# Kernel tuning notes

Measured on AMD Instinct MI355X. Metric: run time of the kernel, lower is better.

The kernel has to match this reference:

```python
import jax, jax.numpy as jnp
import numpy as np

N = 16384   # total nodes per drug-batch
E = 65536   # directed edges (avg degree 4)
B = 512     # graphs per batch
BN_EPS = 1e-5
SLOPE = 0.01  # LeakyReLU default


def _rn(k, shape, s=0.02):
    return jax.random.normal(k, shape, dtype=jnp.float32) * s


def setup_inputs():
    key = jax.random.key(0)
    ks = jax.random.split(key, 32)
    d = {}
    d['x1'] = jax.random.normal(ks[0], (N, 78), dtype=jnp.float32)
    d['edge_index1'] = jax.random.randint(ks[1], (2, E), 0, N)
    d['batch1'] = jnp.sort(jax.random.randint(ks[2], (N,), 0, B))
    d['x2'] = jax.random.normal(ks[3], (N, 78), dtype=jnp.float32)
    d['edge_index2'] = jax.random.randint(ks[4], (2, E), 0, N)
    d['batch2'] = jnp.sort(jax.random.randint(ks[5], (N,), 0, B))
    d['cell'] = jax.random.normal(ks[6], (B, 954), dtype=jnp.float32)
    # TransformerConv1: 78 -> 2 heads x 128 (concat 256)
    d['wq1'] = _rn(ks[7], (78, 256));  d['bq1'] = jnp.zeros((256,), jnp.float32)
    d['wk1'] = _rn(ks[8], (78, 256));  d['bk1'] = jnp.zeros((256,), jnp.float32)
    d['wv1'] = _rn(ks[9], (78, 256));  d['bv1'] = jnp.zeros((256,), jnp.float32)
    d['ws1'] = _rn(ks[10], (78, 256)); d['bs1'] = jnp.zeros((256,), jnp.float32)
    # TransformerConv2: 256 -> 2 heads x 512 (concat 1024)
    d['wq2'] = _rn(ks[11], (256, 1024)); d['bq2'] = jnp.zeros((1024,), jnp.float32)
    d['wk2'] = _rn(ks[12], (256, 1024)); d['bk2'] = jnp.zeros((1024,), jnp.float32)
    d['wv2'] = _rn(ks[13], (256, 1024)); d['bv2'] = jnp.zeros((1024,), jnp.float32)
    d['ws2'] = _rn(ks[14], (256, 1024)); d['bs2'] = jnp.zeros((1024,), jnp.float32)
    d['wg1'] = _rn(ks[15], (1024, 512)); d['bg1'] = jnp.zeros((512,), jnp.float32)
    d['wg2'] = _rn(ks[16], (512, 128));  d['bg2'] = jnp.zeros((128,), jnp.float32)
    d['wr1'] = _rn(ks[17], (954, 512));  d['br1'] = jnp.zeros((512,), jnp.float32)
    d['wr2'] = _rn(ks[18], (512, 256));  d['br2'] = jnp.zeros((256,), jnp.float32)
    d['wr3'] = _rn(ks[19], (256, 128));  d['br3'] = jnp.zeros((128,), jnp.float32)
    d['wf1'] = _rn(ks[20], (384, 512));  d['bf1'] = jnp.zeros((512,), jnp.float32)
    d['gbn1'] = jnp.ones((512,), jnp.float32); d['bbn1'] = jnp.zeros((512,), jnp.float32)
    d['wf2'] = _rn(ks[21], (512, 256));  d['bf2'] = jnp.zeros((256,), jnp.float32)
    d['gbn2'] = jnp.ones((256,), jnp.float32); d['bbn2'] = jnp.zeros((256,), jnp.float32)
    d['wf3'] = _rn(ks[22], (256, 1));    d['bf3'] = jnp.zeros((1,), jnp.float32)
    return d


def _lrelu(x):
    return jnp.where(x >= 0, x, SLOPE * x)


def _l2n(x):
    return x / jnp.maximum(jnp.linalg.norm(x, axis=1, keepdims=True), 1e-12)


def _tconv(x, ei, wq, bq, wk, bk, wv, bv, ws, bs, H, D):
    # PyG TransformerConv (concat=True, beta=False, root_weight=True)
    src, dst = ei[0], ei[1]
    n = x.shape[0]
    q = (x @ wq + bq).reshape(n, H, D)
    k = (x @ wk + bk).reshape(n, H, D)
    v = (x @ wv + bv).reshape(n, H, D)
    logits = jnp.einsum('ehd,ehd->eh', q[dst], k[src]) / jnp.sqrt(jnp.float32(D))  # [E,H]
    m = jax.ops.segment_max(logits, dst, num_segments=n)
    m = jnp.where(jnp.isfinite(m), m, 0.0)
    e = jnp.exp(logits - m[dst])
    z = jax.ops.segment_sum(e, dst, num_segments=n)
    alpha = e / (z[dst] + 1e-16)
    agg = jax.ops.segment_sum(alpha[:, :, None] * v[src], dst, num_segments=n)  # [N,H,D]
    return agg.reshape(n, H * D) + x @ ws + bs


def reference(x1, edge_index1, batch1, x2, edge_index2, batch2, cell,
              wq1, bq1, wk1, bk1, wv1, bv1, ws1, bs1,
              wq2, bq2, wk2, bk2, wv2, bv2, ws2, bs2,
              wg1, bg1, wg2, bg2, wr1, br1, wr2, br2, wr3, br3,
              wf1, bf1, gbn1, bbn1, wf2, bf2, gbn2, bbn2, wf3, bf3):
    def branch(x, ei, bt):
        h = _lrelu(_tconv(x, ei, wq1, bq1, wk1, bk1, wv1, bv1, ws1, bs1, 2, 128))
        h = _lrelu(_tconv(h, ei, wq2, bq2, wk2, bk2, wv2, bv2, ws2, bs2, 2, 512))
        g = jax.ops.segment_max(h, bt, num_segments=B)  # global max pool per graph
        g = jnp.where(jnp.isfinite(g), g, 0.0)
        g = _lrelu(g @ wg1 + bg1)
        g = g @ wg2 + bg2  # dropout = identity in eval
        return _l2n(g)

    x1g = branch(x1, edge_index1, batch1)
    x2g = branch(x2, edge_index2, batch2)

    c = _l2n(cell)
    c = _lrelu(c @ wr1 + br1)
    c = _lrelu(c @ wr2 + br2)
    c = c @ wr3 + br3

    xc = _l2n(jnp.concatenate([x1g, x2g, c], axis=1))  # [B, 384]
    bn = 1.0 / jnp.sqrt(1.0 + BN_EPS)  # eval BN with running mean 0, var 1
    h = _lrelu((xc @ wf1 + bf1) * bn * gbn1 + bbn1)
    h = _lrelu((h @ wf2 + bf2) * bn * gbn2 + bbn2)
    return jax.nn.sigmoid((h @ wf3 + bf3)[:, 0])
```

## Files before the change

### kernel.cpp

```cpp
#include <hip/hip_runtime.h>
#include <hip/hip_bf16.h>
#include <hip/hip_fp8.h>
#include <math.h>
#include <stdint.h>

typedef __hip_bfloat16 bf16;

#define NN 16384
#define EE 65536
#define BB 512

typedef __attribute__((ext_vector_type(8))) short short8;
typedef __attribute__((ext_vector_type(4))) short short4v;
typedef __attribute__((ext_vector_type(4))) float floatx4;
typedef __attribute__((ext_vector_type(8))) unsigned char uchar8;

#define GKEY_NEGINF 0x007FFFFFu

__device__ __forceinline__ float lrelu_f(float x){ return x >= 0.f ? x : 0.01f*x; }

__device__ __forceinline__ float b2f(short s){
    unsigned int u = ((unsigned int)(unsigned short)s) << 16;
    float f; __builtin_memcpy(&f, &u, 4); return f;
}
__device__ __forceinline__ short f2b(float f){
    bf16 b = (bf16)f;
    short s; __builtin_memcpy(&s, &b, 2); return s;
}
__device__ __forceinline__ unsigned char f2fp8(float f){
    __hip_fp8_e4m3 t(f);
    return (unsigned char)t.__x;
}
__device__ __forceinline__ float fp82f(unsigned char c){
    __hip_fp8_e4m3 t; t.__x = (__hip_fp8_storage_t)c;
    return (float)t;
}
__device__ __forceinline__ unsigned int fkey(float f){
    unsigned int u; __builtin_memcpy(&u, &f, 4);
    return (u & 0x80000000u) ? ~u : (u | 0x80000000u);
}
__device__ __forceinline__ float fdec(unsigned int k){
    if (k == GKEY_NEGINF) return 0.f;
    unsigned int u = (k & 0x80000000u) ? (k ^ 0x80000000u) : ~k;
    float f; __builtin_memcpy(&f, &u, 4); return f;
}

__device__ __forceinline__ void gl2lds16(const void* g, void* l){
    __builtin_amdgcn_global_load_lds(
        (__attribute__((address_space(1))) unsigned int*)(uintptr_t)g,
        (__attribute__((address_space(3))) unsigned int*)(uintptr_t)l, 16, 0, 0);
}

__global__ __launch_bounds__(256)
void mfma_gemm(const bf16* __restrict__ A, int lda,
               const bf16* __restrict__ Bt, int ldb,
               const float* __restrict__ bias,
               bf16* __restrict__ C, int ldc,
               unsigned char* __restrict__ C2, int ldc2, int nsplit, int K)
{
    __shared__ __align__(16) char smem[20480];
    bf16* As  = (bf16*)smem;
    bf16* Bs  = (bf16*)(smem + 8192);
    bf16* epi = (bf16*)smem;
    const int tid  = threadIdx.x;
    const int wave = tid >> 6;
    const int lane = tid & 63;
    const int wm = (wave & 1) * 64;
    const int wn = (wave >> 1) * 64;
    const int m0 = blockIdx.y * 128;
    const int n0 = blockIdx.x * 128;
    const bool isf8 = (n0 >= nsplit);

    const int srow = lane >> 2;
    const int scol = (lane & 3) * 8;
    const int arow = lane & 15;
    const int aq   = (lane >> 4) * 8;

    floatx4 acc[4][4];
    #pragma unroll
    for (int i=0;i<4;i++)
        #pragma unroll
        for (int j=0;j<4;j++) acc[i][j] = (floatx4){0.f,0.f,0.f,0.f};

    for (int k0 = 0; k0 < K; k0 += 32) {
        #pragma unroll
        for (int i = 0; i < 2; i++) {
            const int chunk = wave*2 + i;
            const int r = chunk*16 + srow;
            gl2lds16(A  + (size_t)(m0 + r)*lda + k0 + scol, As + chunk*512);
            gl2lds16(Bt + (size_t)(n0 + r)*ldb + k0 + scol, Bs + chunk*512);
        }
        __syncthreads();
        short8 af[4], bf_[4];
        #pragma unroll
        for (int i=0;i<4;i++) af[i]  = *(const short8*)(As + (wm + i*16 + arow)*32 + aq);
        #pragma unroll
        for (int j=0;j<4;j++) bf_[j] = *(const short8*)(Bs + (wn + j*16 + arow)*32 + aq);
        #pragma unroll
        for (int i=0;i<4;i++)
            #pragma unroll
            for (int j=0;j<4;j++)
                acc[i][j] = __builtin_amdgcn_mfma_f32_16x16x32_bf16(af[i], bf_[j], acc[i][j], 0,0,0);
        __syncthreads();
    }
    const int crow = (lane >> 4) * 4;
    const int ccol = lane & 15;
    const int erow = lane >> 2;
    const int ecol = (lane & 3) * 8;
    bf16* ep = epi + wave * (64*40);
    #pragma unroll
    for (int j2 = 0; j2 < 2; j2++){
        if (j2) __syncthreads();
        #pragma unroll
        for (int jj = 0; jj < 2; jj++){
            const int j = j2*2 + jj;
            const float bsv = bias[n0 + wn + j*16 + ccol];
            #pragma unroll
            for (int i = 0; i < 4; i++)
                #pragma unroll
                for (int r = 0; r < 4; r++)
                    ep[(i*16 + crow + r)*40 + jj*16 + ccol] = (bf16)(acc[i][j][r] + bsv);
        }
        __syncthreads();
        #pragma unroll
        for (int q = 0; q < 4; q++){
            const int rr = q*16 + erow;
            short8 vv = *(const short8*)(ep + rr*40 + ecol);
            if (!isf8){
                *(short8*)(C + (size_t)(m0 + wm + rr)*ldc + n0 + wn + j2*32 + ecol) = vv;
            } else {
                uchar8 ob;
                #pragma unroll
                for (int i=0;i<8;i++) ob[i] = f2fp8(b2f(vv[i]));
                *(uchar8*)(C2 + (size_t)(m0 + wm + rr)*ldc2 + (n0 - nsplit) + wn + j2*32 + ecol) = ob;
            }
        }
    }
}

__global__ void prep_all_kernel(const float* __restrict__ wq1, const float* __restrict__ wk1,
                                const float* __restrict__ wv1, const float* __restrict__ ws1,
                                const float* __restrict__ bq1, const float* __restrict__ bk1,
                                const float* __restrict__ bv1, const float* __restrict__ bs1,
                                const float* __restrict__ wq2, const float* __restrict__ wk2,
                                const float* __restrict__ wv2, const float* __restrict__ ws2,
                                const float* __restrict__ bq2, const float* __restrict__ bk2,
                                const float* __restrict__ bv2, const float* __restrict__ bs2v,
                                bf16* __restrict__ W1t, float* __restrict__ b1c,
                                bf16* __restrict__ W2t, float* __restrict__ b2c)
{
    int i = blockIdx.x*256 + threadIdx.x;
    if (i < 98304){
        int n = i / 96, k = i - n*96;
        const float* w = (n<256)?wq1:(n<512)?wk1:(n<768)?wv1:ws1;
        W1t[i] = (k < 78) ? (bf16)w[(size_t)k*256 + (n & 255)] : (bf16)0.f;
        return;
    }
    i -= 98304;
    if (i < 1024){
        const float* b = (i<256)?bq1:(i<512)?bk1:(i<768)?bv1:bs1;
        b1c[i] = b[i & 255];
        return;
    }
    i -= 1024;
    if (i < 1048576){
        int k = i & 255;
        int j = (i >> 8) & 2047;
        int h = i >> 19;
        const float* w = (j<512)?wq2:(j<1024)?ws2:(j<1536)?wk2:wv2;
        int col = h*512 + (j & 511);
        W2t[i] = (bf16)w[(size_t)k*1024 + col];
        return;
    }
    i -= 1048576;
    if (i < 4096){
        int j = i & 2047, h = i >> 11;
        const float* b = (j<512)?bq2:(j<1024)?bs2v:(j<1536)?bk2:bv2;
        b2c[i] = b[h*512 + (j & 511)];
    }
}

#define OG1 0
#define OG2 524288
#define OR1 589824
#define OR2 1081344
#define OR3 1212416
#define OF1 1245184
#define OF2 1441792
#define TAILW_TOTAL 1572864

__global__ void prep_tail_kernel(const float* __restrict__ wg1, const float* __restrict__ wg2,
                                 const float* __restrict__ wr1, const float* __restrict__ wr2,
                                 const float* __restrict__ wr3, const float* __restrict__ wf1,
                                 const float* __restrict__ wf2, bf16* __restrict__ Wtp)
{
    int i = blockIdx.x*256 + threadIdx.x;
    if (i >= TAILW_TOTAL) return;
    const float* W; int N, K, base;
    if      (i < OG2){ W = wg1; N = 512; K = 1024; base = OG1; }
    else if (i < OR1){ W = wg2; N = 128; K = 512;  base = OG2; }
    else if (i < OR2){ W = wr1; N = 512; K = 954;  base = OR1; }
    else if (i < OR3){ W = wr2; N = 256; K = 512;  base = OR2; }
    else if (i < OF1){ W = wr3; N = 128; K = 256;  base = OR3; }
    else if (i < OF2){ W = wf1; N = 512; K = 384;  base = OF1; }
    else             { W = wf2; N = 256; K = 512;  base = OF2; }
    int loc = i - base;
    int u = loc & 3;
    int j = (loc >> 2) % N;
    int k4 = (loc >> 2) / N;
    int k = k4*4 + u;
    Wtp[i] = (k < K) ? (bf16)W[(size_t)k*N + j] : (bf16)0.f;
}

__global__ void cvt_x_kernel(const float* __restrict__ x1, const float* __restrict__ x2,
                             bf16* __restrict__ xa){
    int i = blockIdx.x*256 + threadIdx.x;
    int r = i / 96, c = i - r*96;
    const float* x = (r >= NN) ? x2 : x1;
    int lr = r & (NN-1);
    xa[i] = (c < 78) ? (bf16)x[(size_t)lr*78 + c] : (bf16)0.f;
}

__global__ void hist_kernel(const int* __restrict__ ei1, const int* __restrict__ ei2,
                            int* __restrict__ cnt){
    int eg = blockIdx.x*256 + threadIdx.x;
    int br = eg >> 16, e = eg & (EE-1);
    const int* ei = br ? ei2 : ei1;
    atomicAdd(&cnt[br*NN + ei[EE + e]], 1);
}

__global__ __launch_bounds__(1024)
void scan_kernel(const int* __restrict__ hist, int* __restrict__ rowptr,
                 int* __restrict__ rowcur){
    const int br = blockIdx.x;
    hist   += br*NN;
    rowptr += br*(NN+1);
    rowcur += br*(NN+1);
    __shared__ int sums[1024];
    const int t = threadIdx.x;
    const int base = t*16;
    int loc[16]; int s = 0;
    #pragma unroll
    for (int i=0;i<16;i++){ loc[i]=s; s += hist[base+i]; }
    sums[t] = s; __syncthreads();
    for (int o=1;o<1024;o<<=1){
        int v = (t>=o) ? sums[t-o] : 0;
        __syncthreads();
        sums[t] += v;
        __syncthreads();
    }
    int pref = (t>0) ? sums[t-1] : 0;
    #pragma unroll
    for (int i=0;i<16;i++){
        int v = pref + loc[i];
        rowptr[base+i] = v;
        rowcur[base+i] = v;
    }
    if (t==1023) rowptr[NN] = sums[1023];
}

__global__ void scatter_kernel(const int* __restrict__ ei1, const int* __restrict__ ei2,
                               int* __restrict__ rowcur, int* __restrict__ srcs){
    int eg = blockIdx.x*256 + threadIdx.x;
    int br = eg >> 16, e = eg & (EE-1);
    const int* ei = br ? ei2 : ei1;
    int d = ei[EE + e];
    int pos = atomicAdd(&rowcur[br*(NN+1) + d], 1);
    srcs[br*EE + pos] = ei[e];
}

__global__ void ginit_kernel(unsigned int* __restrict__ gkey){
    gkey[blockIdx.x*256 + threadIdx.x] = GKEY_NEGINF;
}

template<int D>
__global__ __launch_bounds__(256)
void attn_kernel(const bf16* __restrict__ qkvs, int ld, int qo, int ko, int vo, int so, int H,
                 bf16* __restrict__ hout, int ldo,
                 const int* __restrict__ rowptr, const int* __restrict__ srcs)
{
    constexpr int PER = D / 64;
    typedef __attribute__((ext_vector_type(PER))) short shortP;
    const int lane = threadIdx.x & 63;
    const int gw = blockIdx.x * 4 + (threadIdx.x >> 6);
    const int n = gw / H;
    const int h = gw - n*H;
    int br = n >> 14;
    int brNN = br*NN, nl = n - brNN;
    rowptr += br*(NN+1); srcs += br*EE;
    const float qscale = rsqrtf((float)D) * 1.44269504f;
    const int hd = h*D + lane*PER;

    const shortP qv = *(const shortP*)(qkvs + (size_t)n*ld + qo + hd);
    float qr[PER];
    #pragma unroll
    for (int i=0;i<PER;i++) qr[i] = b2f(qv[i]) * qscale;

    const int e0 = rowptr[nl], e1 = rowptr[nl+1];
    float m = -INFINITY, z = 0.f;
    float acc[PER];
    #pragma unroll
    for (int i=0;i<PER;i++) acc[i] = 0.f;

    for (int base = e0; base < e1; base += 4){
        const int cnt = min(4, e1 - base);
        int sl = srcs[min(base + (lane & 3), e1 - 1)];
        int src[4];
        #pragma unroll
        for (int j=0;j<4;j++) src[j] = __shfl(sl, j, 64);

        shortP kv[4], vv[4];
        #pragma unroll
        for (int j=0;j<4;j++){
            if (j < cnt){
                const bf16* rp = qkvs + (size_t)(brNN + src[j])*ld;
                kv[j] = *(const shortP*)(rp + ko + hd);
                vv[j] = *(const shortP*)(rp + vo + hd);
            }
        }
        float dt[4];
        #pragma unroll
        for (int j=0;j<4;j++){
            float d = 0.f;
            if (j < cnt){
                #pragma unroll
                for (int i=0;i<PER;i++) d += qr[i]*b2f(kv[j][i]);
            }
            dt[j] = d;
        }
        #pragma unroll
        for (int o=32;o;o>>=1){
            #pragma unroll
            for (int j=0;j<4;j++) dt[j] += __shfl_xor(dt[j], o, 64);
        }
        float cm = -INFINITY;
        #pragma unroll
        for (int j=0;j<4;j++) if (j < cnt) cm = fmaxf(cm, dt[j]);
        const float mn = fmaxf(m, cm);
        const float cs = exp2f(m - mn);
        z *= cs;
        #pragma unroll
        for (int i=0;i<PER;i++) acc[i] *= cs;
        #pragma unroll
        for (int j=0;j<4;j++){
            if (j < cnt){
                const float w = exp2f(dt[j] - mn);
                z += w;
                #pragma unroll
                for (int i=0;i<PER;i++) acc[i] += w*b2f(vv[j][i]);
            }
        }
        m = mn;
    }
    const float invz = 1.0f/(z + 1e-16f);
    const shortP sv = *(const shortP*)(qkvs + (size_t)n*ld + so + hd);
    shortP ov;
    #pragma unroll
    for (int i=0;i<PER;i++) ov[i] = f2b(lrelu_f(b2f(sv[i]) + acc[i]*invz));
    *(shortP*)(hout + (size_t)n*ldo + hd) = ov;
}

__global__ __launch_bounds__(256)
void attn512_f8(const bf16* __restrict__ qs, const unsigned char* __restrict__ kv,
                const int* __restrict__ rowptr, const int* __restrict__ srcs,
                const int* __restrict__ bt,
                unsigned int* __restrict__ gkey, int grow0, int gc0)
{
    __shared__ float Sh[4][512];
    __shared__ int Sgid[4];
    const int lane = threadIdx.x & 63;
    const int wave = threadIdx.x >> 6;
    const int n = blockIdx.x * 4 + wave;
    const float qscale = rsqrtf(512.f) * 1.44269504f;
    const int hd = lane*8;

    const short8 qv = *(const short8*)(qs + (size_t)n*1024 + hd);
    float qr[8];
    #pragma unroll
    for (int i=0;i<8;i++) qr[i] = b2f(qv[i]) * qscale;

    const int e0 = rowptr[n], e1 = rowptr[n+1];
    float m = -INFINITY, z = 0.f;
    float acc[8];
    #pragma unroll
    for (int i=0;i<8;i++) acc[i] = 0.f;

    for (int base = e0; base < e1; base += 4){
        const int cnt = min(4, e1 - base);
        int sl = srcs[min(base + (lane & 3), e1 - 1)];
        int src[4];
        #pragma unroll
        for (int j=0;j<4;j++) src[j] = __shfl(sl, j, 64);

        uchar8 k8[4], v8[4];
        #pragma unroll
        for (int j=0;j<4;j++){
            if (j < cnt){
                const unsigned char* rp = kv + (size_t)src[j]*1024;
                k8[j] = *(const uchar8*)(rp + hd);
                v8[j] = *(const uchar8*)(rp + 512 + hd);
            }
        }
        float dt[4];
        #pragma unroll
        for (int j=0;j<4;j++){
            float d = 0.f;
            if (j < cnt){
                #pragma unroll
                for (int i=0;i<8;i++) d += qr[i]*fp82f(k8[j][i]);
            }
            dt[j] = d;
        }
        #pragma unroll
        for (int o=32;o;o>>=1){
            #pragma unroll
            for (int j=0;j<4;j++) dt[j] += __shfl_xor(dt[j], o, 64);
        }
        float cm = -INFINITY;
        #pragma unroll
        for (int j=0;j<4;j++) if (j < cnt) cm = fmaxf(cm, dt[j]);
        const float mn = fmaxf(m, cm);
        const float cs = exp2f(m - mn);
        z *= cs;
        #pragma unroll
        for (int i=0;i<8;i++) acc[i] *= cs;
        #pragma unroll
        for (int j=0;j<4;j++){
            if (j < cnt){
                const float w = exp2f(dt[j] - mn);
                z += w;
                #pragma unroll
                for (int i=0;i<8;i++) acc[i] += w*fp82f(v8[j][i]);
            }
        }
        m = mn;
    }
    const float invz = 1.0f/(z + 1e-16f);
    const short8 sv = *(const short8*)(qs + (size_t)n*1024 + 512 + hd);
    #pragma unroll
    for (int i=0;i<8;i++) Sh[wave][hd + i] = lrelu_f(b2f(sv[i]) + acc[i]*invz);
    if (lane == 0) Sgid[wave] = bt[n];
    __syncthreads();

    #pragma unroll
    for (int cc=0; cc<2; cc++){
        const int col = threadIdx.x*2 + cc;
        float mx = Sh[0][col];
        int gid = Sgid[0];
        #pragma unroll
        for (int r=1; r<4; r++){
            if (Sgid[r] == gid) mx = fmaxf(mx, Sh[r][col]);
            else {
                atomicMax(&gkey[(size_t)(grow0 + gid)*1024 + gc0 + col], fkey(mx));
                gid = Sgid[r]; mx = Sh[r][col];
            }
        }
        atomicMax(&gkey[(size_t)(grow0 + gid)*1024 + gc0 + col], fkey(mx));
    }
}

template<int R, int N, int ACT>
__device__ __forceinline__ void dense_split(
    const bf16* __restrict__ Wp, const float* __restrict__ bias,
    const float* __restrict__ gam, const float* __restrict__ bet, float bns,
    const float* A, int lda, float* C, int ldc, int K, int tid, float* Spart)
{
    constexpr int CPT = N / 128;
    constexpr int KG  = 8;
    const int ct = tid & 127;
    const int kg = tid >> 7;
    const int jt = ct * CPT;
    const int Kc = ((K + KG - 1) / KG + 3) & ~3;
    const int kb = kg * Kc;
    const int Kpad = (K + 3) & ~3;
    const int ke = min(Kpad, kb + Kc);

    float acc[R][CPT];
    #pragma unroll
    for (int r=0;r<R;r++)
        #pragma unroll
        for (int c=0;c<CPT;c++) acc[r][c] = 0.f;

    if (kb < ke){
        short8 p0, p1; short4v p4;
        {
            const bf16* wp = Wp + ((size_t)(kb>>2)*N + jt)*4;
            if (CPT==4){ p0 = ((const short8*)wp)[0]; p1 = ((const short8*)wp)[1]; }
            else if (CPT==2){ p0 = *(const short8*)wp; }
            else { p4 = *(const short4v*)wp; }
        }
        for (int k = kb; k < ke; k += 4){
            short8 c0 = p0, c1 = p1; short4v c4 = p4;
            const int kn = (k + 4 < ke) ? k + 4 : kb;
            const bf16* wn = Wp + ((size_t)(kn>>2)*N + jt)*4;
            if (CPT==4){ p0 = ((const short8*)wn)[0]; p1 = ((const short8*)wn)[1]; }
            else if (CPT==2){ p0 = *(const short8*)wn; }
            else { p4 = *(const short4v*)wn; }
            float w[4][CPT];
            if (CPT==4){
                #pragma unroll
                for (int u=0;u<4;u++){
                    w[u][0] = b2f(c0[u]); w[u][1] = b2f(c0[4+u]);
                    w[u][2] = b2f(c1[u]); w[u][3] = b2f(c1[4+u]);
                }
            } else if (CPT==2){
                #pragma unroll
                for (int u=0;u<4;u++){ w[u][0] = b2f(c0[u]); w[u][1] = b2f(c0[4+u]); }
            } else {
                #pragma unroll
                for (int u=0;u<4;u++) w[u][0] = b2f(c4[u]);
            }
            #pragma unroll
            for (int r=0;r<R;r++){
                const floatx4 av = *(const floatx4*)(A + r*lda + k);
                #pragma unroll
                for (int u=0;u<4;u++)
                    #pragma unroll
                    for (int c=0;c<CPT;c++) acc[r][c] += av[u]*w[u][c];
            }
        }
    }
    #pragma unroll
    for (int r=0;r<R;r++)
        #pragma unroll
        for (int c=0;c<CPT;c++)
            Spart[(kg*R + r)*N + jt + c] = acc[r][c];
    __syncthreads();
    for (int idx = tid; idx < R*N; idx += 1024){
        int r = idx / N, j = idx - r*N;
        float v = 0.f;
        #pragma unroll
        for (int g=0; g<KG; g++) v += Spart[(g*R + r)*N + j];
        v += bias[j];
        if (ACT==1) v = lrelu_f(v);
        if (ACT==2) v = lrelu_f(v*bns*gam[j] + bet[j]);
        C[r*ldc + j] = v;
    }
    __syncthreads();
}

__global__ __launch_bounds__(1024)
void tail_kernel(const unsigned int* __restrict__ gkey,
                 const float* __restrict__ cell,
                 const bf16*  __restrict__ Wtp,
                 const float* __restrict__ bg1, const float* __restrict__ bg2,
                 const float* __restrict__ br1, const float* __restrict__ br2,
                 const float* __restrict__ br3,
                 const float* __restrict__ bf1,
                 const float* __restrict__ gbn1, const float* __restrict__ bbn1,
                 const float* __restrict__ bf2,
                 const float* __restrict__ gbn2, const float* __restrict__ bbn2,
                 const float* __restrict__ wf3, const float* __restrict__ bf3,
                 float bns, float* __restrict__ outp)
{
    __shared__ float Sg[4][1024];
    __shared__ float Sgh[4][512];
    __shared__ float Sgout[4][128];
    __shared__ float Scell[2][960];
    __shared__ float Sc1[2][512];
    __shared__ float Sc2[2][256];
    __shared__ float Sc3[2][128];
    __shared__ float Sxc[2][384];
    __shared__ float Sf1[2][512];
    __shared__ float Sf2[2][256];
    __shared__ float Spart[16384];
    __shared__ float inv4[4], invc[2], invx[2];

    const int tid = threadIdx.x;
    const int wv  = tid >> 6;
    const int ln  = tid & 63;
    const int b0  = blockIdx.x * 2;

    {
        int idx = tid*4;
        int r = idx >> 10, c = idx & 1023;
        int lg = r >> 1, br = r & 1;
        const unsigned int* gp = gkey + (size_t)(br*BB + b0 + lg)*1024 + c;
        #pragma unroll
        for (int i=0;i<4;i++) Sg[r][c+i] = fdec(gp[i]);
    }
    for (int idx = tid; idx < 2*954; idx += 1024){
        int r = (idx >= 954) ? 1 : 0;
        int c = idx - r*954;
        Scell[r][c] = cell[(size_t)(b0 + r)*954 + c];
    }
    if (tid < 12){ int r = tid/6; Scell[r][954 + tid%6] = 0.f; }
    __syncthreads();

    if (wv < 2){
        float s = 0.f;
        for (int c = ln; c < 954; c += 64){ float v = Scell[wv][c]; s += v*v; }
        #pragma unroll
        for (int o=32;o;o>>=1) s += __shfl_xor(s, o, 64);
        if (ln == 0) invc[wv] = 1.0f / fmaxf(sqrtf(s), 1e-12f);
    }
    __syncthreads();
    #pragma unroll
    for (int r=0;r<2;r++)
        for (int c = tid; c < 954; c += 1024) Scell[r][c] *= invc[r];
    __syncthreads();

    dense_split<4,512,1>(Wtp+OG1, bg1, nullptr, nullptr, 1.f, &Sg[0][0],   1024, &Sgh[0][0],  512, 1024, tid, Spart);
    dense_split<4,128,0>(Wtp+OG2, bg2, nullptr, nullptr, 1.f, &Sgh[0][0],  512,  &Sgout[0][0],128, 512,  tid, Spart);
    dense_split<2,512,1>(Wtp+OR1, br1, nullptr, nullptr, 1.f, &Scell[0][0], 960, &Sc1[0][0],  512, 954,  tid, Spart);
    dense_split<2,256,1>(Wtp+OR2, br2, nullptr, nullptr, 1.f, &Sc1[0][0],   512, &Sc2[0][0],  256, 512,  tid, Spart);
    dense_split<2,128,0>(Wtp+OR3, br3, nullptr, nullptr, 1.f, &Sc2[0][0],   256, &Sc3[0][0],  128, 256,  tid, Spart);

    if (wv < 4){
        float a = Sgout[wv][ln], bq = Sgout[wv][ln+64];
        float s = a*a + bq*bq;
        #pragma unroll
        for (int o=32;o;o>>=1) s += __shfl_xor(s, o, 64);
        if (ln == 0) inv4[wv] = 1.0f / fmaxf(sqrtf(s), 1e-12f);
    }
    __syncthreads();

    if (tid < 768){
        int lg = tid / 384, j = tid - lg*384;
        float v;
        if (j < 128)      v = Sgout[lg*2+0][j]     * inv4[lg*2+0];
        else if (j < 256) v = Sgout[lg*2+1][j-128] * inv4[lg*2+1];
        else              v = Sc3[lg][j-256];
        Sxc[lg][j] = v;
    }
    __syncthreads();
    if (wv < 2){
        float s = 0.f;
        #pragma unroll
        for (int i=0;i<6;i++){ float v = Sxc[wv][ln + i*64]; s += v*v; }
        #pragma unroll
        for (int o=32;o;o>>=1) s += __shfl_xor(s, o, 64);
        if (ln == 0) invx[wv] = 1.0f / fmaxf(sqrtf(s), 1e-12f);
    }
    __syncthreads();
    if (tid < 768){
        int lg = tid / 384, j = tid - lg*384;
        Sxc[lg][j] *= invx[lg];
    }
    __syncthreads();

    dense_split<2,512,2>(Wtp+OF1, bf1, gbn1, bbn1, bns, &Sxc[0][0], 384, &Sf1[0][0], 512, 384, tid, Spart);
    dense_split<2,256,2>(Wtp+OF2, bf2, gbn2, bbn2, bns, &Sf1[0][0], 512, &Sf2[0][0], 256, 512, tid, Spart);

    if (wv < 2){
        float s = 0.f;
        #pragma unroll
        for (int i=0;i<4;i++){ int c = ln + i*64; s += Sf2[wv][c]*wf3[c]; }
        #pragma unroll
        for (int o=32;o;o>>=1) s += __shfl_xor(s, o, 64);
        if (ln == 0) outp[b0 + wv] = 1.0f/(1.0f + expf(-(s + bf3[0])));
    }
}

extern "C" void kernel_launch(void* const* d_in, const int* in_sizes, int n_in,
                              void* d_out, int out_size, void* d_ws, size_t ws_size,
                              hipStream_t stream)
{
    const float* x1  = (const float*)d_in[0];
    const int*   ei1 = (const int*)  d_in[1];
    const int*   bt1 = (const int*)  d_in[2];
    const float* x2  = (const float*)d_in[3];
    const int*   ei2 = (const int*)  d_in[4];
    const int*   bt2 = (const int*)  d_in[5];
    const float* cell= (const float*)d_in[6];
    const float* wq1=(const float*)d_in[7];  const float* bq1=(const float*)d_in[8];
    const float* wk1=(const float*)d_in[9];  const float* bk1=(const float*)d_in[10];
    const float* wv1=(const float*)d_in[11]; const float* bv1=(const float*)d_in[12];
    const float* ws1=(const float*)d_in[13]; const float* bs1=(const float*)d_in[14];
    const float* wq2=(const float*)d_in[15]; const float* bq2=(const float*)d_in[16];
    const float* wk2=(const float*)d_in[17]; const float* bk2=(const float*)d_in[18];
    const float* wv2=(const float*)d_in[19]; const float* bv2=(const float*)d_in[20];
    const float* ws2=(const float*)d_in[21]; const float* bs2q=(const float*)d_in[22];
    const float* wg1=(const float*)d_in[23]; const float* bg1=(const float*)d_in[24];
    const float* wg2=(const float*)d_in[25]; const float* bg2=(const float*)d_in[26];
    const float* wr1=(const float*)d_in[27]; const float* br1=(const float*)d_in[28];
    const float* wr2=(const float*)d_in[29]; const float* br2=(const float*)d_in[30];
    const float* wr3=(const float*)d_in[31]; const float* br3=(const float*)d_in[32];
    const float* wf1=(const float*)d_in[33]; const float* bf1=(const float*)d_in[34];
    const float* gbn1=(const float*)d_in[35];const float* bbn1=(const float*)d_in[36];
    const float* wf2=(const float*)d_in[37]; const float* bf2=(const float*)d_in[38];
    const float* gbn2=(const float*)d_in[39];const float* bbn2=(const float*)d_in[40];
    const float* wf3=(const float*)d_in[41]; const float* bf3=(const float*)d_in[42];
    float* outp = (float*)d_out;
    (void)in_sizes; (void)n_in; (void)out_size; (void)ws_size;

    const float BNS = 1.0f / sqrtf(1.0f + 1e-5f);

    char* basep = (char*)d_ws;
    size_t off = 0;
    auto alloc = [&](size_t nbytes)->char* {
        char* p = basep + off;
        off += (nbytes + 255) & ~(size_t)255;
        return p;
    };
    int* rowptr2  = (int*)  alloc((size_t)2*(NN+1)*4);
    int* rowcur2  = (int*)  alloc((size_t)2*(NN+1)*4);
    int* cnt2     = (int*)  alloc((size_t)2*NN*4);
    int* srcs2    = (int*)  alloc((size_t)2*EE*4);
    unsigned int* gkey = (unsigned int*)alloc((size_t)2*BB*1024*4);
    float* b1c    = (float*)alloc((size_t)1024*4);
    float* b2c    = (float*)alloc((size_t)4096*4);
    bf16* W1t     = (bf16*) alloc((size_t)1024*96*2);
    bf16* W2t     = (bf16*) alloc((size_t)2*2048*256*2);
    bf16* Wtp     = (bf16*) alloc((size_t)TAILW_TOTAL*2);
    bf16* h1      = (bf16*) alloc((size_t)2*NN*256*2);
    bf16* xa      = (bf16*) alloc((size_t)2*NN*96*2);
    char* QK      = alloc((size_t)2*NN*1024*2);
    bf16* qkvs1   = (bf16*)QK;
    bf16* qs2     = (bf16*)QK;
    unsigned char* kv2 = (unsigned char*)(QK + (size_t)NN*1024*2);

    (void)hipMemsetAsync(cnt2, 0, (size_t)2*NN*4, stream);
    prep_all_kernel<<<4500,256,0,stream>>>(wq1,wk1,wv1,ws1, bq1,bk1,bv1,bs1,
                                           wq2,wk2,wv2,ws2, bq2,bk2,bv2,bs2q,
                                           W1t,b1c,W2t,b2c);
    prep_tail_kernel<<<(TAILW_TOTAL+255)/256,256,0,stream>>>(wg1,wg2,wr1,wr2,wr3,wf1,wf2, Wtp);
    hist_kernel<<<2*EE/256,256,0,stream>>>(ei1, ei2, cnt2);
    scan_kernel<<<2,1024,0,stream>>>(cnt2, rowptr2, rowcur2);
    scatter_kernel<<<2*EE/256,256,0,stream>>>(ei1, ei2, rowcur2, srcs2);
    ginit_kernel<<<(2*BB*1024)/256,256,0,stream>>>(gkey);

    cvt_x_kernel<<<(2*NN*96)/256,256,0,stream>>>(x1, x2, xa);
    mfma_gemm<<<dim3(1024/128, 2*NN/128),256,0,stream>>>(xa,96, W1t,96, b1c,
                                                         qkvs1,1024, nullptr,0, 1<<30, 96);
    attn_kernel<128><<<2*NN*2/4,256,0,stream>>>(qkvs1,1024, 0,256,512,768, 2, h1,256, rowptr2, srcs2);

    for (int br=0; br<2; br++){
        const int* bt = br ? bt2 : bt1;
        for (int h=0; h<2; h++){
            mfma_gemm<<<dim3(2048/128, NN/128),256,0,stream>>>(
                h1 + (size_t)br*NN*256, 256, W2t + (size_t)h*2048*256, 256,
                b2c + h*2048, qs2,1024, kv2,1024, 1024, 256);
            attn512_f8<<<NN/4,256,0,stream>>>(qs2, kv2,
                                              rowptr2 + br*(NN+1), srcs2 + br*EE, bt,
                                              gkey, br*BB, h*512);
        }
    }

    tail_kernel<<<BB/2,1024,0,stream>>>(gkey, cell, Wtp,
                                        bg1,bg2, br1,br2,br3,
                                        bf1,gbn1,bbn1, bf2,gbn2,bbn2, wf3,bf3,
                                        BNS, outp);
}
```

Before: 560.4 us.

## Store layer-1 Q/K/V in fp8, reorder skip first, merge prep kernels

Reorders the projected columns so the skip projection is written in bf16 and Q/K/V are written in fp8 by the GEMM epilogue for both layers, including layer 1 which previously stayed all-bf16. The attention kernels now read fp8 queries, keys and values, which cuts gather bandwidth. All weight, input conversion and gkey-init prep kernels are merged into one launch to reduce launch overhead. The cost is reduced precision on Q (and on layer-1 K/V), which risks accuracy.

```diff
diff --git a/kernel.cpp b/kernel.cpp
--- a/kernel.cpp
+++ b/kernel.cpp
@@ -12,8 +12,10 @@
 
 typedef __attribute__((ext_vector_type(8))) short short8;
 typedef __attribute__((ext_vector_type(4))) short short4v;
+typedef __attribute__((ext_vector_type(2))) short short2v;
 typedef __attribute__((ext_vector_type(4))) float floatx4;
 typedef __attribute__((ext_vector_type(8))) unsigned char uchar8;
+typedef __attribute__((ext_vector_type(2))) unsigned char uchar2v;
 
 #define GKEY_NEGINF 0x007FFFFFu
 
@@ -138,48 +140,6 @@
     }
 }
 
-__global__ void prep_all_kernel(const float* __restrict__ wq1, const float* __restrict__ wk1,
-                                const float* __restrict__ wv1, const float* __restrict__ ws1,
-                                const float* __restrict__ bq1, const float* __restrict__ bk1,
-                                const float* __restrict__ bv1, const float* __restrict__ bs1,
-                                const float* __restrict__ wq2, const float* __restrict__ wk2,
-                                const float* __restrict__ wv2, const float* __restrict__ ws2,
-                                const float* __restrict__ bq2, const float* __restrict__ bk2,
-                                const float* __restrict__ bv2, const float* __restrict__ bs2v,
-                                bf16* __restrict__ W1t, float* __restrict__ b1c,
-                                bf16* __restrict__ W2t, float* __restrict__ b2c)
-{
-    int i = blockIdx.x*256 + threadIdx.x;
-    if (i < 98304){
-        int n = i / 96, k = i - n*96;
-        const float* w = (n<256)?wq1:(n<512)?wk1:(n<768)?wv1:ws1;
-        W1t[i] = (k < 78) ? (bf16)w[(size_t)k*256 + (n & 255)] : (bf16)0.f;
-        return;
-    }
-    i -= 98304;
-    if (i < 1024){
-        const float* b = (i<256)?bq1:(i<512)?bk1:(i<768)?bv1:bs1;
-        b1c[i] = b[i & 255];
-        return;
-    }
-    i -= 1024;
-    if (i < 1048576){
-        int k = i & 255;
-        int j = (i >> 8) & 2047;
-        int h = i >> 19;
-        const float* w = (j<512)?wq2:(j<1024)?ws2:(j<1536)?wk2:wv2;
-        int col = h*512 + (j & 511);
-        W2t[i] = (bf16)w[(size_t)k*1024 + col];
-        return;
-    }
-    i -= 1048576;
-    if (i < 4096){
-        int j = i & 2047, h = i >> 11;
-        const float* b = (j<512)?bq2:(j<1024)?bs2v:(j<1536)?bk2:bv2;
-        b2c[i] = b[h*512 + (j & 511)];
-    }
-}
-
 #define OG1 0
 #define OG2 524288
 #define OR1 589824
@@ -189,36 +149,92 @@
 #define OF2 1441792
 #define TAILW_TOTAL 1572864
 
-__global__ void prep_tail_kernel(const float* __restrict__ wg1, const float* __restrict__ wg2,
-                                 const float* __restrict__ wr1, const float* __restrict__ wr2,
-                                 const float* __restrict__ wr3, const float* __restrict__ wf1,
-                                 const float* __restrict__ wf2, bf16* __restrict__ Wtp)
+#define P_W1T 98304
+#define P_B1C (P_W1T + 1024)
+#define P_W2T (P_B1C + 1048576)
+#define P_B2C (P_W2T + 4096)
+#define P_WTP (P_B2C + TAILW_TOTAL)
+#define P_XA  (P_WTP + 2*NN*96)
+#define P_GK  (P_XA + 2*BB*1024)
+__global__ void prep_mega_kernel(
+    const float* __restrict__ wq1, const float* __restrict__ wk1,
+    const float* __restrict__ wv1, const float* __restrict__ ws1,
+    const float* __restrict__ bq1, const float* __restrict__ bk1,
+    const float* __restrict__ bv1, const float* __restrict__ bs1,
+    const float* __restrict__ wq2, const float* __restrict__ wk2,
+    const float* __restrict__ wv2, const float* __restrict__ ws2,
+    const float* __restrict__ bq2, const float* __restrict__ bk2,
+    const float* __restrict__ bv2, const float* __restrict__ bs2v,
+    const float* __restrict__ wg1, const float* __restrict__ wg2,
+    const float* __restrict__ wr1, const float* __restrict__ wr2,
+    const float* __restrict__ wr3, const float* __restrict__ wf1,
+    const float* __restrict__ wf2,
+    const float* __restrict__ x1,  const float* __restrict__ x2,
+    bf16* __restrict__ W1t, float* __restrict__ b1c,
+    bf16* __restrict__ W2t, float* __restrict__ b2c,
+    bf16* __restrict__ Wtp, bf16* __restrict__ xa,
+    unsigned int* __restrict__ gkey)
 {
     int i = blockIdx.x*256 + threadIdx.x;
-    if (i >= TAILW_TOTAL) return;
-    const float* W; int N, K, base;
-    if      (i < OG2){ W = wg1; N = 512; K = 1024; base = OG1; }
-    else if (i < OR1){ W = wg2; N = 128; K = 512;  base = OG2; }
-    else if (i < OR2){ W = wr1; N = 512; K = 954;  base = OR1; }
-    else if (i < OR3){ W = wr2; N = 256; K = 512;  base = OR2; }
-    else if (i < OF1){ W = wr3; N = 128; K = 256;  base = OR3; }
-    else if (i < OF2){ W = wf1; N = 512; K = 384;  base = OF1; }
-    else             { W = wf2; N = 256; K = 512;  base = OF2; }
-    int loc = i - base;
-    int u = loc & 3;
-    int j = (loc >> 2) % N;
-    int k4 = (loc >> 2) / N;
-    int k = k4*4 + u;
-    Wtp[i] = (k < K) ? (bf16)W[(size_t)k*N + j] : (bf16)0.f;
-}
-
-__global__ void cvt_x_kernel(const float* __restrict__ x1, const float* __restrict__ x2,
-                             bf16* __restrict__ xa){
-    int i = blockIdx.x*256 + threadIdx.x;
-    int r = i / 96, c = i - r*96;
-    const float* x = (r >= NN) ? x2 : x1;
-    int lr = r & (NN-1);
-    xa[i] = (c < 78) ? (bf16)x[(size_t)lr*78 + c] : (bf16)0.f;
+    if (i < P_W1T){
+        int n = i / 96, k = i - n*96;
+        int seg = n >> 8;
+        const float* w = (seg==0)?ws1:(seg==1)?wq1:(seg==2)?wk1:wv1;
+        W1t[i] = (k < 78) ? (bf16)w[(size_t)k*256 + (n & 255)] : (bf16)0.f;
+        return;
+    }
+    if (i < P_B1C){
+        int n = i - P_W1T;
+        int seg = n >> 8;
+        const float* b = (seg==0)?bs1:(seg==1)?bq1:(seg==2)?bk1:bv1;
+        b1c[n] = b[n & 255];
+        return;
+    }
+    if (i < P_W2T){
+        int loc = i - P_B1C;
+        int k = loc & 255;
+        int j = (loc >> 8) & 2047;
+        int h = loc >> 19;
+        const float* w = (j<512)?ws2:(j<1024)?wq2:(j<1536)?wk2:wv2;
+        W2t[loc] = (bf16)w[(size_t)k*1024 + h*512 + (j & 511)];
+        return;
+    }
+    if (i < P_B2C){
+        int loc = i - P_W2T;
+        int j = loc & 2047, h = loc >> 11;
+        const float* b = (j<512)?bs2v:(j<1024)?bq2:(j<1536)?bk2:bv2;
+        b2c[loc] = b[h*512 + (j & 511)];
+        return;
+    }
+    if (i < P_WTP){
+        int t = i - P_B2C;
+        const float* W; int N, K, base;
+        if      (t < OG2){ W = wg1; N = 512; K = 1024; base = OG1; }
+        else if (t < OR1){ W = wg2; N = 128; K = 512;  base = OG2; }
+        else if (t < OR2){ W = wr1; N = 512; K = 954;  base = OR1; }
+        else if (t < OR3){ W = wr2; N = 256; K = 512;  base = OR2; }
+        else if (t < OF1){ W = wr3; N = 128; K = 256;  base = OR3; }
+        else if (t < OF2){ W = wf1; N = 512; K = 384;  base = OF1; }
+        else             { W = wf2; N = 256; K = 512;  base = OF2; }
+        int loc = t - base;
+        int u = loc & 3;
+        int j = (loc >> 2) % N;
+        int k4 = (loc >> 2) / N;
+        int k = k4*4 + u;
+        Wtp[t] = (k < K) ? (bf16)W[(size_t)k*N + j] : (bf16)0.f;
+        return;
+    }
+    if (i < P_XA){
+        int t = i - P_WTP;
+        int r = t / 96, c = t - r*96;
+        const float* x = (r >= NN) ? x2 : x1;
+        int lr = r & (NN-1);
+        xa[t] = (c < 78) ? (bf16)x[(size_t)lr*78 + c] : (bf16)0.f;
+        return;
+    }
+    if (i < P_GK){
+        gkey[i - P_XA] = GKEY_NEGINF;
+    }
 }
 
 __global__ void hist_kernel(const int* __restrict__ ei1, const int* __restrict__ ei2,
@@ -269,38 +285,27 @@
     srcs[br*EE + pos] = ei[e];
 }
 
-__global__ void ginit_kernel(unsigned int* __restrict__ gkey){
-    gkey[blockIdx.x*256 + threadIdx.x] = GKEY_NEGINF;
-}
-
-template<int D>
 __global__ __launch_bounds__(256)
-void attn_kernel(const bf16* __restrict__ qkvs, int ld, int qo, int ko, int vo, int so, int H,
-                 bf16* __restrict__ hout, int ldo,
-                 const int* __restrict__ rowptr, const int* __restrict__ srcs)
+void attn128_f8(const bf16* __restrict__ s1, const unsigned char* __restrict__ f81,
+                bf16* __restrict__ hout,
+                const int* __restrict__ rowptr, const int* __restrict__ srcs)
 {
-    constexpr int PER = D / 64;
-    typedef __attribute__((ext_vector_type(PER))) short shortP;
     const int lane = threadIdx.x & 63;
     const int gw = blockIdx.x * 4 + (threadIdx.x >> 6);
-    const int n = gw / H;
-    const int h = gw - n*H;
+    const int n = gw >> 1;
+    const int h = gw & 1;
     int br = n >> 14;
     int brNN = br*NN, nl = n - brNN;
     rowptr += br*(NN+1); srcs += br*EE;
-    const float qscale = rsqrtf((float)D) * 1.44269504f;
-    const int hd = h*D + lane*PER;
-
-    const shortP qv = *(const shortP*)(qkvs + (size_t)n*ld + qo + hd);
-    float qr[PER];
-    #pragma unroll
-    for (int i=0;i<PER;i++) qr[i] = b2f(qv[i]) * qscale;
+    const float qscale = rsqrtf(128.f) * 1.44269504f;
+    const int hd = h*128 + lane*2;
+
+    const uchar2v q8 = *(const uchar2v*)(f81 + (size_t)n*768 + hd);
+    float qr[2] = { fp82f(q8[0])*qscale, fp82f(q8[1])*qscale };
 
     const int e0 = rowptr[nl], e1 = rowptr[nl+1];
     float m = -INFINITY, z = 0.f;
-    float acc[PER];
-    #pragma unroll
-    for (int i=0;i<PER;i++) acc[i] = 0.f;
+    float acc[2] = {0.f, 0.f};
 
     for (int base = e0; base < e1; base += 4){
         const int cnt = min(4, e1 - base);
@@ -309,23 +314,20 @@
         #pragma unroll
         for (int j=0;j<4;j++) src[j] = __shfl(sl, j, 64);
 
-        shortP kv[4], vv[4];
+        uchar2v kv[4], vv[4];
         #pragma unroll
         for (int j=0;j<4;j++){
             if (j < cnt){
-                const bf16* rp = qkvs + (size_t)(brNN + src[j])*ld;
-                kv[j] = *(const shortP*)(rp + ko + hd);
-                vv[j] = *(const shortP*)(rp + vo + hd);
+                const unsigned char* rp = f81 + (size_t)(brNN + src[j])*768;
+                kv[j] = *(const uchar2v*)(rp + 256 + hd);
+                vv[j] = *(const uchar2v*)(rp + 512 + hd);
             }
         }
         float dt[4];
         #pragma unroll
         for (int j=0;j<4;j++){
             float d = 0.f;
-            if (j < cnt){
-                #pragma unroll
-                for (int i=0;i<PER;i++) d += qr[i]*b2f(kv[j][i]);
-            }
+            if (j < cnt) d = qr[0]*fp82f(kv[j][0]) + qr[1]*fp82f(kv[j][1]);
             dt[j] = d;
         }
         #pragma unroll
@@ -339,29 +341,28 @@
         const float mn = fmaxf(m, cm);
         const float cs = exp2f(m - mn);
         z *= cs;
-        #pragma unroll
-        for (int i=0;i<PER;i++) acc[i] *= cs;
+        acc[0] *= cs; acc[1] *= cs;
         #pragma unroll
         for (int j=0;j<4;j++){
             if (j < cnt){
                 const float w = exp2f(dt[j] - mn);
                 z += w;
-                #pragma unroll
-                for (int i=0;i<PER;i++) acc[i] += w*b2f(vv[j][i]);
+                acc[0] += w*fp82f(vv[j][0]);
+                acc[1] += w*fp82f(vv[j][1]);
             }
         }
         m = mn;
     }
     const float invz = 1.0f/(z + 1e-16f);
-    const shortP sv = *(const shortP*)(qkvs + (size_t)n*ld + so + hd);
-    shortP ov;
-    #pragma unroll
-    for (int i=0;i<PER;i++) ov[i] = f2b(lrelu_f(b2f(sv[i]) + acc[i]*invz));
-    *(shortP*)(hout + (size_t)n*ldo + hd) = ov;
+    const short2v sv = *(const short2v*)(s1 + (size_t)n*256 + hd);
+    short2v ov;
+    ov[0] = f2b(lrelu_f(b2f(sv[0]) + acc[0]*invz));
+    ov[1] = f2b(lrelu_f(b2f(sv[1]) + acc[1]*invz));
+    *(short2v*)(hout + (size_t)n*256 + hd) = ov;
 }
 
 __global__ __launch_bounds__(256)
-void attn512_f8(const bf16* __restrict__ qs, const unsigned char* __restrict__ kv,
+void attn512_f8(const bf16* __restrict__ s2, const unsigned char* __restrict__ f82,
                 const int* __restrict__ rowptr, const int* __restrict__ srcs,
                 const int* __restrict__ bt,
                 unsigned int* __restrict__ gkey, int grow0, int gc0)
@@ -374,10 +375,10 @@
     const float qscale = rsqrtf(512.f) * 1.44269504f;
     const int hd = lane*8;
 
-    const short8 qv = *(const short8*)(qs + (size_t)n*1024 + hd);
+    const uchar8 q8 = *(const uchar8*)(f82 + (size_t)n*1536 + hd);
     float qr[8];
     #pragma unroll
-    for (int i=0;i<8;i++) qr[i] = b2f(qv[i]) * qscale;
+    for (int i=0;i<8;i++) qr[i] = fp82f(q8[i]) * qscale;
 
     const int e0 = rowptr[n], e1 = rowptr[n+1];
     float m = -INFINITY, z = 0.f;
@@ -396,9 +397,9 @@
         #pragma unroll
         for (int j=0;j<4;j++){
             if (j < cnt){
-                const unsigned char* rp = kv + (size_t)src[j]*1024;
-                k8[j] = *(const uchar8*)(rp + hd);
-                v8[j] = *(const uchar8*)(rp + 512 + hd);
+                const unsigned char* rp = f82 + (size_t)src[j]*1536;
+                k8[j] = *(const uchar8*)(rp + 512 + hd);
+                v8[j] = *(const uchar8*)(rp + 1024 + hd);
             }
         }
         float dt[4];
@@ -436,7 +437,7 @@
         m = mn;
     }
     const float invz = 1.0f/(z + 1e-16f);
-    const short8 sv = *(const short8*)(qs + (size_t)n*1024 + 512 + hd);
+    const short8 sv = *(const short8*)(s2 + (size_t)n*512 + hd);
     #pragma unroll
     for (int i=0;i<8;i++) Sh[wave][hd + i] = lrelu_f(b2f(sv[i]) + acc[i]*invz);
     if (lane == 0) Sgid[wave] = bt[n];
@@ -705,33 +706,34 @@
     bf16* Wtp     = (bf16*) alloc((size_t)TAILW_TOTAL*2);
     bf16* h1      = (bf16*) alloc((size_t)2*NN*256*2);
     bf16* xa      = (bf16*) alloc((size_t)2*NN*96*2);
-    char* QK      = alloc((size_t)2*NN*1024*2);
-    bf16* qkvs1   = (bf16*)QK;
-    bf16* qs2     = (bf16*)QK;
-    unsigned char* kv2 = (unsigned char*)(QK + (size_t)NN*1024*2);
+    char* QK      = alloc((size_t)16777216 + 25165824);
+    bf16* s1a     = (bf16*)QK;
+    unsigned char* f81 = (unsigned char*)(QK + 16777216);
+    bf16* s2a     = (bf16*)QK;
+    unsigned char* f82 = (unsigned char*)(QK + 16777216);
 
     (void)hipMemsetAsync(cnt2, 0, (size_t)2*NN*4, stream);
-    prep_all_kernel<<<4500,256,0,stream>>>(wq1,wk1,wv1,ws1, bq1,bk1,bv1,bs1,
-                                           wq2,wk2,wv2,ws2, bq2,bk2,bv2,bs2q,
-                                           W1t,b1c,W2t,b2c);
-    prep_tail_kernel<<<(TAILW_TOTAL+255)/256,256,0,stream>>>(wg1,wg2,wr1,wr2,wr3,wf1,wf2, Wtp);
+    prep_mega_kernel<<<P_GK/256,256,0,stream>>>(
+        wq1,wk1,wv1,ws1, bq1,bk1,bv1,bs1,
+        wq2,wk2,wv2,ws2, bq2,bk2,bv2,bs2q,
+        wg1,wg2,wr1,wr2,wr3,wf1,wf2,
+        x1,x2,
+        W1t,b1c,W2t,b2c, Wtp, xa, gkey);
     hist_kernel<<<2*EE/256,256,0,stream>>>(ei1, ei2, cnt2);
     scan_kernel<<<2,1024,0,stream>>>(cnt2, rowptr2, rowcur2);
     scatter_kernel<<<2*EE/256,256,0,stream>>>(ei1, ei2, rowcur2, srcs2);
-    ginit_kernel<<<(2*BB*1024)/256,256,0,stream>>>(gkey);
-
-    cvt_x_kernel<<<(2*NN*96)/256,256,0,stream>>>(x1, x2, xa);
-    mfma_gemm<<<dim3(1024/128, 2*NN/128),256,0,stream>>>(xa,96, W1t,96, b1c,
-                                                         qkvs1,1024, nullptr,0, 1<<30, 96);
-    attn_kernel<128><<<2*NN*2/4,256,0,stream>>>(qkvs1,1024, 0,256,512,768, 2, h1,256, rowptr2, srcs2);
+
+    mfma_gemm<<<dim3(8, 2*NN/128),256,0,stream>>>(xa,96, W1t,96, b1c,
+                                                  s1a,256, f81,768, 256, 96);
+    attn128_f8<<<2*NN*2/4,256,0,stream>>>(s1a, f81, h1, rowptr2, srcs2);
 
     for (int br=0; br<2; br++){
         const int* bt = br ? bt2 : bt1;
         for (int h=0; h<2; h++){
-            mfma_gemm<<<dim3(2048/128, NN/128),256,0,stream>>>(
+            mfma_gemm<<<dim3(16, NN/128),256,0,stream>>>(
                 h1 + (size_t)br*NN*256, 256, W2t + (size_t)h*2048*256, 256,
-                b2c + h*2048, qs2,1024, kv2,1024, 1024, 256);
-            attn512_f8<<<NN/4,256,0,stream>>>(qs2, kv2,
+                b2c + h*2048, s2a,512, f82,1536, 512, 256);
+            attn512_f8<<<NN/4,256,0,stream>>>(s2a, f82,
                                               rowptr2 + br*(NN+1), srcs2 + br*EE, bt,
                                               gkey, br*BB, h*512);
         }
```

Result: no change. 555.4 us (-0.9%).
